# Optimization experiments

Measured on AMD Instinct MI355X. Metric: run time of the kernel, lower is better.

## Reference

```python
import jax, jax.numpy as jnp
import numpy as np

N_HEADS = 16
HEAD_SIZE = 64
N_EMB = 1024
BLOCK = 2048
B, T = 2, 2048

def setup_inputs() -> dict:
    key = jax.random.key(0)
    ks = jax.random.split(key, 6)
    s = 0.02
    x = jax.random.normal(ks[0], (B, T, N_EMB), dtype=jnp.float32)
    # per-head projection weights, stacked: [H, C, hs] (no bias, per module)
    Wq = jax.random.normal(ks[1], (N_HEADS, N_EMB, HEAD_SIZE), dtype=jnp.float32) * s
    Wk = jax.random.normal(ks[2], (N_HEADS, N_EMB, HEAD_SIZE), dtype=jnp.float32) * s
    Wv = jax.random.normal(ks[3], (N_HEADS, N_EMB, HEAD_SIZE), dtype=jnp.float32) * s
    # output projection: Linear(n_heads*head_size -> n_embedding), with bias
    Wo = jax.random.normal(ks[4], (N_HEADS * HEAD_SIZE, N_EMB), dtype=jnp.float32) * s
    bo = jax.random.normal(ks[5], (N_EMB,), dtype=jnp.float32) * s
    return {"x": x, "Wq": Wq, "Wk": Wk, "Wv": Wv, "Wo": Wo, "bo": bo}

def reference(x, Wq, Wk, Wv, Wo, bo):
    # x: [B,T,C]; projections per head -> [B,H,T,hs]
    q = jnp.einsum('btc,hcd->bhtd', x, Wq)
    k = jnp.einsum('btc,hcd->bhtd', x, Wk)
    v = jnp.einsum('btc,hcd->bhtd', x, Wv)
    scale = 1.0 / jnp.sqrt(jnp.asarray(HEAD_SIZE, dtype=x.dtype))
    scores = jnp.einsum('bhtd,bhsd->bhts', q, k) * scale  # [B,H,T,T]
    Tq = x.shape[1]
    causal = jnp.tril(jnp.ones((Tq, Tq), dtype=bool))
    scores = jnp.where(causal, scores, jnp.asarray(-jnp.inf, dtype=scores.dtype))
    attn = jax.nn.softmax(scores, axis=-1)  # dropout in eval mode (identity)
    out = jnp.einsum('bhts,bhsd->bhtd', attn, v)  # [B,H,T,hs]
    # concat heads along last dim (matches torch.cat order over head list)
    out = out.transpose(0, 2, 1, 3).reshape(x.shape[0], Tq, N_HEADS * HEAD_SIZE)
    return out @ Wo + bo
```

## Files before the change

### kernel.cpp

```cpp
#include <hip/hip_runtime.h>


typedef short v8s __attribute__((ext_vector_type(8)));
typedef float v4f __attribute__((ext_vector_type(4)));

#define DEVI __device__ __forceinline__

#define B_SZ 2
#define T_SEQ 2048
#define NH 16
#define HS 64
#define CEMB 1024
#define MROWS (B_SZ * T_SEQ)
#define KSZ 1024
#define SCALE_Q 0.18033688011112042f

DEVI unsigned short f2bf(float f) {
  union { float f; unsigned u; } c; c.f = f;
  unsigned u = c.u;
  unsigned r = (u + 0x7FFFu + ((u >> 16) & 1u)) >> 16;
  return (unsigned short)r;
}

DEVI float exp2_fast(float x) {
  float r;
  asm("v_exp_f32 %0, %1" : "=v"(r) : "v"(x));
  return r;
}

DEVI unsigned cvt_pk_bf16(float lo, float hi) {
  unsigned r;
  asm("v_cvt_pk_bf16_f32 %0, %1, %2" : "=v"(r) : "v"(lo), "v"(hi));
  return r;
}

DEVI void gload_lds16(const void* g, void* l) {
  __builtin_amdgcn_global_load_lds(
      (const __attribute__((address_space(1))) void*)g,
      (__attribute__((address_space(3))) void*)l, 16, 0, 0);
}

__global__ void cvt_f32_bf16x4(const float* __restrict__ in,
                               unsigned short* __restrict__ out, int n4) {
  int i = blockIdx.x * blockDim.x + threadIdx.x;
  if (i >= n4) return;
  float4 v = ((const float4*)in)[i];
  ushort4 o;
  o.x = f2bf(v.x); o.y = f2bf(v.y); o.z = f2bf(v.z); o.w = f2bf(v.w);
  ((ushort4*)out)[i] = o;
}

__global__ void transpose_cvt(const float* __restrict__ in,
                              unsigned short* __restrict__ out, int R, int C) {
  __shared__ float tile[32][33];
  size_t zoff = (size_t)blockIdx.z * R * C;
  in += zoff; out += zoff;
  int c0 = blockIdx.x * 32, r0 = blockIdx.y * 32;
  int tx = threadIdx.x, ty = threadIdx.y;
#pragma unroll
  for (int j = 0; j < 4; ++j) {
    int r = r0 + ty + j * 8;
    tile[ty + j * 8][tx] = in[(size_t)r * C + c0 + tx];
  }
  __syncthreads();
#pragma unroll
  for (int j = 0; j < 4; ++j) {
    int c = c0 + ty + j * 8;
    out[(size_t)c * R + r0 + tx] = f2bf(tile[tx][ty + j * 8]);
  }
}

template <int MODE>
__global__ __launch_bounds__(256, 4) void gemm_bt(
    const unsigned short* __restrict__ A, const unsigned short* __restrict__ Bt,
    void* __restrict__ Cout, const float* __restrict__ bias) {
  __shared__ __align__(16) unsigned short As[2][128 * 32];
  __shared__ __align__(16) unsigned short Bs[2][128 * 32];

  const int tid = threadIdx.x;
  const int lane = tid & 63, w = tid >> 6;
  const int wm = w >> 1, wn = w & 1;
  const int lr = lane & 15, lg = lane >> 4;
  const int mb = blockIdx.y * 128, nb = blockIdx.x * 128;

  v4f acc[4][4];
  v4f zero = {0.f, 0.f, 0.f, 0.f};
#pragma unroll
  for (int i = 0; i < 4; ++i)
#pragma unroll
    for (int j = 0; j < 4; ++j) acc[i][j] = zero;

  const int srow = lane >> 2;
  const int sgcol = ((lane & 3) ^ (srow & 3)) * 8;
  const unsigned short* gA = A + (size_t)(mb + w * 32 + srow) * KSZ + sgcol;
  const unsigned short* gB = Bt + (size_t)(nb + w * 32 + srow) * KSZ + sgcol;
  unsigned short* lA = &As[0][0] + w * 1024;
  unsigned short* lB = &Bs[0][0] + w * 1024;

#define STAGE_G(cur, kb)                                    \
  do {                                                      \
    gload_lds16(gA + (kb), lA + (cur) * 4096);              \
    gload_lds16(gA + (kb) + 16 * KSZ, lA + (cur) * 4096 + 512); \
    gload_lds16(gB + (kb), lB + (cur) * 4096);              \
    gload_lds16(gB + (kb) + 16 * KSZ, lB + (cur) * 4096 + 512); \
  } while (0)

  STAGE_G(0, 0);
  __syncthreads();
  int cur = 0;

  for (int kb = 0; kb < KSZ; kb += 32) {
    if (kb + 32 < KSZ) STAGE_G(cur ^ 1, kb + 32);
    v8s af[4], bfr[4];
#pragma unroll
    for (int i = 0; i < 4; ++i) {
      int ra = wm * 64 + i * 16 + lr, rb = wn * 64 + i * 16 + lr;
      af[i]  = *(const v8s*)&As[cur][ra * 32 + ((lg ^ (lr & 3)) << 3)];
      bfr[i] = *(const v8s*)&Bs[cur][rb * 32 + ((lg ^ (lr & 3)) << 3)];
    }
#pragma unroll
    for (int i = 0; i < 4; ++i)
#pragma unroll
      for (int j = 0; j < 4; ++j)
        acc[i][j] = __builtin_amdgcn_mfma_f32_16x16x32_bf16(af[i], bfr[j], acc[i][j], 0, 0, 0);
    __syncthreads();
    cur ^= 1;
  }
#undef STAGE_G

#pragma unroll
  for (int i = 0; i < 4; ++i) {
    int mrow0 = mb + wm * 64 + i * 16 + lg * 4;
#pragma unroll
    for (int j = 0; j < 4; ++j) {
      int ncol = nb + wn * 64 + j * 16 + lr;
      if (MODE == 0) {
        int p = ncol >> 10, rem = ncol & 1023, h = rem >> 6, d = rem & 63;
        float sc = (p == 0) ? SCALE_Q : 1.0f;
        unsigned short* out = (unsigned short*)Cout;
#pragma unroll
        for (int r = 0; r < 4; ++r) {
          int mrow = mrow0 + r;
          int b = mrow >> 11, t = mrow & 2047;
          size_t off;
          if (p < 2)
            off = ((size_t)((p * B_SZ + b) * NH + h) * T_SEQ + t) * HS + d;
          else
            off = (size_t)(2 * B_SZ * NH) * T_SEQ * HS +
                  ((size_t)(b * NH + h) * HS + d) * T_SEQ + t;
          out[off] = f2bf(acc[i][j][r] * sc);
        }
      } else {
        float* out = (float*)Cout;
        float bv = bias[ncol];
#pragma unroll
        for (int r = 0; r < 4; ++r)
          out[(size_t)(mrow0 + r) * CEMB + ncol] = acc[i][j][r] + bv;
      }
    }
  }
}

__global__ __launch_bounds__(512, 4) void attn_kernel(
    const unsigned short* __restrict__ Qg, const unsigned short* __restrict__ Kg,
    const unsigned short* __restrict__ Vtg, unsigned short* __restrict__ Yg) {
  __shared__ __align__(16) unsigned char lds[64 * 1024];
  unsigned char* KsB = lds;
  unsigned char* VtB = lds + 16384;
  unsigned char* PsB = lds + 32768;

  const int tid = threadIdx.x;
  const int lane = tid & 63, w = tid >> 6;
  const int lr = lane & 15, lg = lane >> 4;
  const int qc = 15 - (blockIdx.x >> 5);
  const int bh = blockIdx.x & 31;

  const unsigned short* Qbase = Qg + (size_t)bh * T_SEQ * HS;
  const unsigned short* Kbase = Kg + (size_t)bh * T_SEQ * HS;
  const unsigned short* Vtbase = Vtg + (size_t)bh * T_SEQ * HS;

  const int ks_row = tid >> 3, ks_cb = tid & 7;
  const int kLds0 = ks_row * 128 + ((ks_cb ^ (ks_row & 7)) << 4);
  const int vs_d = tid >> 4, vs_sc = tid & 15;
  const int vLds0 = vs_d * 256 + ((vs_sc ^ (vs_d & 15)) << 4);
  const unsigned short* Kg0 = Kbase + ks_row * HS + ks_cb * 8;
  const unsigned short* Vg0 = Vtbase + (size_t)vs_d * T_SEQ + vs_sc * 8;

  v8s qA[2];
  {
    const unsigned short* qrow = Qbase + (size_t)(qc * 128 + w * 16 + lr) * HS;
    qA[0] = *(const v8s*)(qrow + lg * 8);
    qA[1] = *(const v8s*)(qrow + 32 + lg * 8);
  }

  v4f O[4];
  v4f zero = {0.f, 0.f, 0.f, 0.f};
#pragma unroll
  for (int d = 0; d < 4; ++d) O[d] = zero;
  float mrun = -1e30f, lrun = 0.f;

  unsigned char* PsW = PsB + w * 4096;

  int4 gK0 = *(const int4*)(Kg0);
  int4 gK1 = *(const int4*)(Kg0 + 4096);
  int4 gV0 = *(const int4*)(Vg0);
  int4 gV1 = *(const int4*)(Vg0 + 32 * T_SEQ);

  for (int t = 0; t <= qc; ++t) {
    __syncthreads();
    *(int4*)(KsB + kLds0) = gK0;
    *(int4*)(KsB + kLds0 + 8192) = gK1;
    *(int4*)(VtB + vLds0) = gV0;
    *(int4*)(VtB + vLds0 + 8192) = gV1;
    __syncthreads();
    if (t < qc) {
      const unsigned short* kp = Kg0 + (t + 1) * (128 * HS);
      gK0 = *(const int4*)kp;
      gK1 = *(const int4*)(kp + 4096);
      const unsigned short* vp = Vg0 + (t + 1) * 128;
      gV0 = *(const int4*)vp;
      gV1 = *(const int4*)(vp + 32 * T_SEQ);
    }

    const int cflim = (t == qc) ? w : 7;
    const int k2lim = (t == qc) ? (w >> 1) : 3;

    v4f S[8];
#pragma unroll
    for (int cf = 0; cf < 8; ++cf) {
      if (cf <= cflim) {
        S[cf] = zero;
#pragma unroll
        for (int ks = 0; ks < 2; ++ks) {
          int srow = cf * 16 + lr;
          v8s kb = *(const v8s*)(KsB + srow * 128 +
                                 ((((ks << 2) + lg) ^ (lr & 7)) << 4));
          S[cf] = __builtin_amdgcn_mfma_f32_16x16x32_bf16(kb, qA[ks], S[cf], 0, 0, 0);
        }
      } else {
        S[cf] = (v4f){-1e30f, -1e30f, -1e30f, -1e30f};
      }
    }

    if (t == qc) {
#pragma unroll
      for (int cf = 0; cf < 8; ++cf)
        if (cf == w) {
#pragma unroll
          for (int r = 0; r < 4; ++r)
            if (lg * 4 + r > lr) S[cf][r] = -1e30f;
        }
    }

    float mx = -1e30f;
#pragma unroll
    for (int cf = 0; cf < 8; ++cf)
#pragma unroll
      for (int r = 0; r < 4; ++r) mx = fmaxf(mx, S[cf][r]);
    mx = fmaxf(mx, __shfl_xor(mx, 16));
    mx = fmaxf(mx, __shfl_xor(mx, 32));
    float mn = fmaxf(mrun, mx);
    float alpha = exp2_fast(mrun - mn);
    mrun = mn;
    float sum = 0.f;
#pragma unroll
    for (int cf = 0; cf < 8; ++cf)
#pragma unroll
      for (int r = 0; r < 4; ++r) {
        float p = exp2_fast(S[cf][r] - mn);
        S[cf][r] = p;
        sum += p;
      }
    sum += __shfl_xor(sum, 16);
    sum += __shfl_xor(sum, 32);
    lrun = lrun * alpha + sum;
#pragma unroll
    for (int df = 0; df < 4; ++df)
#pragma unroll
      for (int r = 0; r < 4; ++r) O[df][r] *= alpha;

#pragma unroll
    for (int cf = 0; cf < 8; ++cf) {
      unsigned d0 = cvt_pk_bf16(S[cf][0], S[cf][1]);
      unsigned d1 = cvt_pk_bf16(S[cf][2], S[cf][3]);
      int c16 = 2 * cf + (lg >> 1);
      unsigned char* p = PsW + lr * 256 + ((c16 ^ lr) << 4) + ((lg & 1) << 3);
      *(unsigned*)p = d0;
      *(unsigned*)(p + 4) = d1;
    }

#pragma unroll
    for (int k2 = 0; k2 < 4; ++k2) {
      if (k2 <= k2lim) {
        v8s pa = *(const v8s*)(PsW + lr * 256 + ((((k2 << 2) + lg) ^ lr) << 4));
#pragma unroll
        for (int df = 0; df < 4; ++df) {
          int d = df * 16 + lr;
          v8s vb = *(const v8s*)(VtB + d * 256 + ((((k2 << 2) + lg) ^ lr) << 4));
          O[df] = __builtin_amdgcn_mfma_f32_16x16x32_bf16(vb, pa, O[df], 0, 0, 0);
        }
      }
    }
  }

  float invl = 1.0f / lrun;
  int tq = qc * 128 + w * 16 + lr;
  int b = bh >> 4, h = bh & 15;
  size_t ybase = ((size_t)b * T_SEQ + tq) * (NH * HS) + h * 64;
#pragma unroll
  for (int df = 0; df < 4; ++df) {
    ushort4 o4;
    o4.x = f2bf(O[df][0] * invl);
    o4.y = f2bf(O[df][1] * invl);
    o4.z = f2bf(O[df][2] * invl);
    o4.w = f2bf(O[df][3] * invl);
    *(ushort4*)(Yg + ybase + df * 16 + lg * 4) = o4;
  }
}

extern "C" void kernel_launch(void* const* d_in, const int* in_sizes, int n_in,
                              void* d_out, int out_size, void* d_ws, size_t ws_size,
                              hipStream_t stream) {
  (void)in_sizes; (void)n_in; (void)out_size; (void)ws_size;
  const float* x  = (const float*)d_in[0];
  const float* Wq = (const float*)d_in[1];
  const float* Wk = (const float*)d_in[2];
  const float* Wv = (const float*)d_in[3];
  const float* Wo = (const float*)d_in[4];
  const float* bo = (const float*)d_in[5];

  unsigned char* ws = (unsigned char*)d_ws;
  unsigned short* xb  = (unsigned short*)(ws);
  unsigned short* Wt  = (unsigned short*)(ws + (8u << 20));
  unsigned short* Wot = (unsigned short*)(ws + (14u << 20));
  unsigned short* qkv = (unsigned short*)(ws + (16u << 20));
  unsigned short* Y   = (unsigned short*)(ws + (40u << 20));

  cvt_f32_bf16x4<<<4096, 256, 0, stream>>>(x, xb, (MROWS * CEMB) / 4);

  dim3 tb(32, 8);
  transpose_cvt<<<dim3(2, 32, 16), tb, 0, stream>>>(Wq, Wt, 1024, 64);
  transpose_cvt<<<dim3(2, 32, 16), tb, 0, stream>>>(Wk, Wt + (1u << 20), 1024, 64);
  transpose_cvt<<<dim3(2, 32, 16), tb, 0, stream>>>(Wv, Wt + (2u << 20), 1024, 64);
  transpose_cvt<<<dim3(32, 32, 1), tb, 0, stream>>>(Wo, Wot, 1024, 1024);

  gemm_bt<0><<<dim3(24, 32), 256, 0, stream>>>(xb, Wt, qkv, nullptr);

  const unsigned short* Qp = qkv;
  const unsigned short* Kp = qkv + (size_t)B_SZ * NH * T_SEQ * HS;
  const unsigned short* Vtp = qkv + (size_t)2 * B_SZ * NH * T_SEQ * HS;
  attn_kernel<<<dim3(512), 512, 0, stream>>>(Qp, Kp, Vtp, Y);

  gemm_bt<1><<<dim3(8, 32), 256, 0, stream>>>(Y, Wot, d_out, bo);
}
```

Measured before the change: 120.6 us.

## Triple-buffer GEMM LDS stages with explicit vmcnt waits and barriers

Moves the projection GEMM from double to triple buffering of the A and B tiles in LDS. Three k-stages are prefetched up front. Each iteration waits with s_waitcnt vmcnt(8) and a raw barrier, runs the MFMAs, then refills the buffer it just consumed, so global loads can run further ahead of the math. LDS use rises by half, and launch bounds drop to 3 blocks per CU. The fixed vmcnt(8) may not wait for the needed stage in the last two iterations, when fewer loads are outstanding, which risks reading data that has not landed yet.

```diff
diff --git a/kernel.cpp b/kernel.cpp
--- a/kernel.cpp
+++ b/kernel.cpp
@@ -71,11 +71,11 @@
 }
 
 template <int MODE>
-__global__ __launch_bounds__(256, 4) void gemm_bt(
+__global__ __launch_bounds__(256, 3) void gemm_bt(
     const unsigned short* __restrict__ A, const unsigned short* __restrict__ Bt,
     void* __restrict__ Cout, const float* __restrict__ bias) {
-  __shared__ __align__(16) unsigned short As[2][128 * 32];
-  __shared__ __align__(16) unsigned short Bs[2][128 * 32];
+  __shared__ __align__(16) unsigned short As[3][128 * 32];
+  __shared__ __align__(16) unsigned short Bs[3][128 * 32];
 
   const int tid = threadIdx.x;
   const int lane = tid & 63, w = tid >> 6;
@@ -97,34 +97,40 @@
   unsigned short* lA = &As[0][0] + w * 1024;
   unsigned short* lB = &Bs[0][0] + w * 1024;
 
-#define STAGE_G(cur, kb)                                    \
-  do {                                                      \
-    gload_lds16(gA + (kb), lA + (cur) * 4096);              \
-    gload_lds16(gA + (kb) + 16 * KSZ, lA + (cur) * 4096 + 512); \
-    gload_lds16(gB + (kb), lB + (cur) * 4096);              \
-    gload_lds16(gB + (kb) + 16 * KSZ, lB + (cur) * 4096 + 512); \
+#define STAGE_G(buf, kb)                                        \
+  do {                                                          \
+    gload_lds16(gA + (kb), lA + (buf) * 4096);                  \
+    gload_lds16(gA + (kb) + 16 * KSZ, lA + (buf) * 4096 + 512); \
+    gload_lds16(gB + (kb), lB + (buf) * 4096);                  \
+    gload_lds16(gB + (kb) + 16 * KSZ, lB + (buf) * 4096 + 512); \
   } while (0)
 
   STAGE_G(0, 0);
-  __syncthreads();
-  int cur = 0;
-
-  for (int kb = 0; kb < KSZ; kb += 32) {
-    if (kb + 32 < KSZ) STAGE_G(cur ^ 1, kb + 32);
+  STAGE_G(1, 32);
+  STAGE_G(2, 64);
+
+  const int NT = KSZ / 32;
+  for (int t = 0; t < NT; ++t) {
+    asm volatile("s_waitcnt vmcnt(8)" ::: "memory");
+    __builtin_amdgcn_s_barrier();
+
+    const int buf = t % 3;
     v8s af[4], bfr[4];
 #pragma unroll
     for (int i = 0; i < 4; ++i) {
       int ra = wm * 64 + i * 16 + lr, rb = wn * 64 + i * 16 + lr;
-      af[i]  = *(const v8s*)&As[cur][ra * 32 + ((lg ^ (lr & 3)) << 3)];
-      bfr[i] = *(const v8s*)&Bs[cur][rb * 32 + ((lg ^ (lr & 3)) << 3)];
+      af[i]  = *(const v8s*)&As[buf][ra * 32 + ((lg ^ (lr & 3)) << 3)];
+      bfr[i] = *(const v8s*)&Bs[buf][rb * 32 + ((lg ^ (lr & 3)) << 3)];
     }
 #pragma unroll
     for (int i = 0; i < 4; ++i)
 #pragma unroll
       for (int j = 0; j < 4; ++j)
         acc[i][j] = __builtin_amdgcn_mfma_f32_16x16x32_bf16(af[i], bfr[j], acc[i][j], 0, 0, 0);
-    __syncthreads();
-    cur ^= 1;
+
+    asm volatile("s_waitcnt lgkmcnt(0)" ::: "memory");
+    __builtin_amdgcn_s_barrier();
+    if (t + 3 < NT) STAGE_G(buf, (t + 3) * 32);
   }
 #undef STAGE_G
 
```

After: 124.4 us. +3.1%, slower.
